# Kernel tuning notes

Hardware: AMD Instinct MI355X
Metric: run time of the kernel (lower is better)

## Reference

```python
import jax, jax.numpy as jnp
import numpy as np
from jax import lax

C = 512   # n_feat == Cn == Cdim (forced by DA_conv/CA_layer consistency)
H, W = 16, 32  # reshape_codebooks(512)
K = 3     # kernel_size
RED = 8   # reduction


def _lrelu(x):
    return jax.nn.leaky_relu(x, 0.1)


def _conv1x1(x, w, b=None):
    # x: (B,C,H,W), w: (O,C) -- torch Conv2d(.,.,1) weight squeezed
    y = jnp.einsum('oc,bchw->bohw', w, x)
    if b is not None:
        y = y + b[None, :, None, None]
    return y


def _conv3x3(x, w, b):
    # x: (B,C,H,W), w: (O,C,3,3) OIHW, padding=k//2 == SAME for odd k
    y = lax.conv_general_dilated(x, w, (1, 1), 'SAME',
                                 dimension_numbers=('NCHW', 'OIHW', 'NCHW'))
    return y + b[None, :, None, None]


def _da_conv(c, deg, kw1, kw2, pw, pb, caw1, caw2):
    # per-channel dynamic kernels from degradation vectors: (Cn, K*K)
    kern = (_lrelu(deg @ kw1.T) @ kw2.T).reshape(C, 1, K, K)
    # depthwise conv, groups = b1*c1 = C (b1 == 1)
    out = lax.conv_general_dilated(c, kern, (1, 1), 'SAME',
                                   feature_group_count=C,
                                   dimension_numbers=('NCHW', 'OIHW', 'NCHW'))
    out = _lrelu(out)
    out = _conv1x1(out, pw, pb)
    # CA_layer: deg reshaped to (1, Cn, 16, 32), channel attention, deg * att
    dr = deg.reshape(1, C, H, W)
    att = jax.nn.sigmoid(_conv1x1(_lrelu(_conv1x1(dr, caw1)), caw2))
    return out + dr * att


def setup_inputs() -> dict:
    key = jax.random.key(0)
    ks = jax.random.split(key, 16)
    n = lambda i, shape, s=0.05: jax.random.normal(ks[i], shape, dtype=jnp.float32) * s
    return dict(
        c=jax.random.normal(ks[0], (1, C, H, W), dtype=jnp.float32),
        deg=jax.random.normal(ks[1], (C, C), dtype=jnp.float32) * 0.1,
        k1_w1=n(2, (C, C)), k1_w2=n(3, (K * K, C)),
        p1_w=n(4, (C, C)), p1_b=jnp.zeros((C,), jnp.float32),
        ca1_w1=n(5, (C // RED, C)), ca1_w2=n(6, (C, C // RED)),
        conv1_w=n(7, (C, C, K, K)), conv1_b=jnp.zeros((C,), jnp.float32),
        k2_w1=n(8, (C, C)), k2_w2=n(9, (K * K, C)),
        p2_w=n(10, (C, C)), p2_b=jnp.zeros((C,), jnp.float32),
        ca2_w1=n(11, (C // RED, C)), ca2_w2=n(12, (C, C // RED)),
        conv2_w=n(13, (C, C, K, K)), conv2_b=jnp.zeros((C,), jnp.float32),
    )


def reference(c, deg, k1_w1, k1_w2, p1_w, p1_b, ca1_w1, ca1_w2,
              conv1_w, conv1_b, k2_w1, k2_w2, p2_w, p2_b,
              ca2_w1, ca2_w2, conv2_w, conv2_b):
    out = _lrelu(_da_conv(c, deg, k1_w1, k1_w2, p1_w, p1_b, ca1_w1, ca1_w2))
    out = _lrelu(_conv3x3(out, conv1_w, conv1_b))
    out = _lrelu(_da_conv(out, deg, k2_w1, k2_w2, p2_w, p2_b, ca2_w1, ca2_w2))
    return _conv3x3(out, conv2_w, conv2_b) + c
```

## Files before the change

kernel.cpp:

```cpp
#include <hip/hip_runtime.h>
#include <hip/hip_bf16.h>

typedef __attribute__((ext_vector_type(8))) unsigned short ushort8;
typedef __attribute__((ext_vector_type(8))) __bf16 bf16x8;
typedef __attribute__((ext_vector_type(4))) float f32x4;
typedef __attribute__((ext_vector_type(4))) unsigned short ushort4v;

__device__ __forceinline__ float lrelu_f(float v){ return v > 0.f ? v : 0.1f*v; }

__device__ __forceinline__ unsigned short f2bf(float v){
  unsigned u = __float_as_uint(v);
  unsigned r = (u + 0x7fffu + ((u>>16)&1u)) >> 16;
  return (unsigned short)r;
}
__device__ __forceinline__ float bf2f(unsigned short u){
  return __uint_as_float(((unsigned)u)<<16);
}

__device__ __forceinline__ void packq(const float* __restrict__ s,
                                      unsigned short* __restrict__ d, int i){
  const float4 v = ((const float4*)s)[i];
  ushort4v o; o.x=f2bf(v.x); o.y=f2bf(v.y); o.z=f2bf(v.z); o.w=f2bf(v.w);
  *(ushort4v*)(d + (size_t)i*4) = o;
}

__global__ __launch_bounds__(256) void k_pack_all(
  const float* __restrict__ k1_w1, const float* __restrict__ k2_w1,
  const float* __restrict__ p1_w,  const float* __restrict__ p2_w,
  const float* __restrict__ ca1_w1,const float* __restrict__ ca1_w2,
  const float* __restrict__ ca2_w1,const float* __restrict__ ca2_w2,
  const float* __restrict__ deg,   const float* __restrict__ conv1_w,
  const float* __restrict__ conv2_w,
  unsigned short* __restrict__ K1B, unsigned short* __restrict__ K2B,
  unsigned short* __restrict__ P1B, unsigned short* __restrict__ P2B,
  unsigned short* __restrict__ CA1A,unsigned short* __restrict__ CA1B,
  unsigned short* __restrict__ CA2A,unsigned short* __restrict__ CA2B,
  unsigned short* __restrict__ DEGB,unsigned short* __restrict__ DEGT,
  unsigned short* __restrict__ WB1, unsigned short* __restrict__ WB2){
  int i = blockIdx.x*256 + threadIdx.x;
  if (i < 65536){ packq(k1_w1, K1B, i); return; } i -= 65536;
  if (i < 65536){ packq(k2_w1, K2B, i); return; } i -= 65536;
  if (i < 65536){ packq(p1_w,  P1B, i); return; } i -= 65536;
  if (i < 65536){ packq(p2_w,  P2B, i); return; } i -= 65536;
  if (i < 8192){ packq(ca1_w1, CA1A, i); return; } i -= 8192;
  if (i < 8192){ packq(ca1_w2, CA1B, i); return; } i -= 8192;
  if (i < 8192){ packq(ca2_w1, CA2A, i); return; } i -= 8192;
  if (i < 8192){ packq(ca2_w2, CA2B, i); return; } i -= 8192;
  if (i < 65536){ packq(deg, DEGB, i); return; } i -= 65536;
  if (i < 65536){
    const int j = i*4; const int p = j>>9, c = j&511;
    ushort4v o;
    o.x = f2bf(deg[(size_t)(c+0)*512 + p]);
    o.y = f2bf(deg[(size_t)(c+1)*512 + p]);
    o.z = f2bf(deg[(size_t)(c+2)*512 + p]);
    o.w = f2bf(deg[(size_t)(c+3)*512 + p]);
    *(ushort4v*)(DEGT + (size_t)j) = o;
    return;
  } i -= 65536;
  if (i < 589824){
    const int o_ = i/1152; const int r4 = (i - o_*1152)*4;
    const int t = r4>>9; const int ci = r4&511;
    const float* s = conv1_w + (size_t)o_*4608;
    ushort4v o;
    o.x = f2bf(s[(ci+0)*9 + t]); o.y = f2bf(s[(ci+1)*9 + t]);
    o.z = f2bf(s[(ci+2)*9 + t]); o.w = f2bf(s[(ci+3)*9 + t]);
    *(ushort4v*)(WB1 + (size_t)o_*4608 + r4) = o;
    return;
  } i -= 589824;
  if (i < 589824){
    const int o_ = i/1152; const int r4 = (i - o_*1152)*4;
    const int t = r4>>9; const int ci = r4&511;
    const float* s = conv2_w + (size_t)o_*4608;
    ushort4v o;
    o.x = f2bf(s[(ci+0)*9 + t]); o.y = f2bf(s[(ci+1)*9 + t]);
    o.z = f2bf(s[(ci+2)*9 + t]); o.w = f2bf(s[(ci+3)*9 + t]);
    *(ushort4v*)(WB2 + (size_t)o_*4608 + r4) = o;
  }
}

__device__ __forceinline__ void gemm64(
    const unsigned short* __restrict__ A, const unsigned short* __restrict__ Bt,
    int m0, int n0, int K, int tid,
    unsigned short* lA, unsigned short* lB, f32x4 acc[2][2]){
  const int wid = tid>>6, lane = tid&63;
  const int srow = tid>>2, skb = tid&3;
  const unsigned short* gA = A  + (size_t)(m0+srow)*K + skb*8;
  const unsigned short* gB = Bt + (size_t)(n0+srow)*K + skb*8;
  const int soff = srow*32 + 8*(skb ^ (srow&3));
  const int wr = (wid>>1)*32, wc = (wid&1)*32;
  const int l15 = lane&15, lkb = lane>>4;
  int aoff[2], boff[2];
  #pragma unroll
  for (int s=0;s<2;s++){
    const int Ra = wr + s*16 + l15;
    aoff[s] = Ra*32 + 8*(lkb ^ (Ra&3));
    const int Rb = wc + s*16 + l15;
    boff[s] = Rb*32 + 8*(lkb ^ (Rb&3));
  }
  const int nst = K>>5;
  ushort8 ra = *(const ushort8*)gA;
  ushort8 rb = *(const ushort8*)gB;
  *(ushort8*)(lA + soff) = ra;
  *(ushort8*)(lB + soff) = rb;
  if (nst > 1){ ra = *(const ushort8*)(gA+32); rb = *(const ushort8*)(gB+32); }
  __syncthreads();
  for (int st=0; st<nst; ++st){
    const int cur = (st&1)*2048;
    bf16x8 af[2], bfr[2];
    #pragma unroll
    for (int s=0;s<2;s++){
      af[s]  = *(const bf16x8*)(lA + cur + aoff[s]);
      bfr[s] = *(const bf16x8*)(lB + cur + boff[s]);
    }
    if (st+1 < nst){
      const int nxt = ((st+1)&1)*2048;
      *(ushort8*)(lA + nxt + soff) = ra;
      *(ushort8*)(lB + nxt + soff) = rb;
      if (st+2 < nst){
        ra = *(const ushort8*)(gA + (size_t)(st+2)*32);
        rb = *(const ushort8*)(gB + (size_t)(st+2)*32);
      }
    }
    #pragma unroll
    for (int mi=0;mi<2;mi++)
      #pragma unroll
      for (int ni=0;ni<2;ni++)
        acc[mi][ni] = __builtin_amdgcn_mfma_f32_16x16x32_bf16(af[mi], bfr[ni], acc[mi][ni], 0,0,0);
    __syncthreads();
  }
}

__global__ __launch_bounds__(256) void k_mgemm_pre(
    const unsigned short* __restrict__ DEGB, const unsigned short* __restrict__ DEGT,
    const unsigned short* __restrict__ K1B,  const unsigned short* __restrict__ K2B,
    const unsigned short* __restrict__ CA1A, const unsigned short* __restrict__ CA2A,
    float* __restrict__ TMP1, float* __restrict__ TMP2,
    unsigned short* __restrict__ HID1, unsigned short* __restrict__ HID2){
  const int z = blockIdx.z;
  if (z >= 2 && blockIdx.y != 0) return;
  const unsigned short* A  = (z < 2) ? DEGB : DEGT;
  const unsigned short* Bt = (z==0) ? K1B : (z==1) ? K2B : (z==2) ? CA1A : CA2A;
  __shared__ unsigned short lA[4096], lB[4096];
  const int tid = threadIdx.x;
  const int m0 = blockIdx.x*64, n0 = blockIdx.y*64;
  f32x4 acc[2][2] = {};
  gemm64(A, Bt, m0, n0, 512, tid, lA, lB, acc);

  const int wid = tid>>6, lane = tid&63;
  const int wr = (wid>>1)*32, wc = (wid&1)*32;
  const int l15 = lane&15, lkb = lane>>4;
  #pragma unroll
  for (int mi=0;mi<2;mi++)
    #pragma unroll
    for (int ni=0;ni<2;ni++){
      const int row = m0 + wr + mi*16 + lkb*4;
      const int col = n0 + wc + ni*16 + l15;
      #pragma unroll
      for (int r=0;r<4;r++){
        const float v = lrelu_f(acc[mi][ni][r]);
        if (z==0)      TMP1[(size_t)(row+r)*512 + col] = v;
        else if (z==1) TMP2[(size_t)(row+r)*512 + col] = v;
        else if (z==2) HID1[(size_t)(row+r)*64 + col] = f2bf(v);
        else           HID2[(size_t)(row+r)*64 + col] = f2bf(v);
      }
    }
}

__global__ __launch_bounds__(256) void k_kern_att(
    const float* __restrict__ TMP1, const float* __restrict__ TMP2,
    const float* __restrict__ kw2a, const float* __restrict__ kw2b,
    const unsigned short* __restrict__ CA1B, const unsigned short* __restrict__ CA2B,
    const unsigned short* __restrict__ HID1, const unsigned short* __restrict__ HID2,
    float* __restrict__ kern0, float* __restrict__ kern1,
    float* __restrict__ ATT1, float* __restrict__ ATT2){
  const int z = blockIdx.z;
  const int tid = threadIdx.x;
  if (z < 2){
    const float* tmp  = z ? TMP2 : TMP1;
    const float* kw2  = z ? kw2b : kw2a;
    float* kern       = z ? kern1 : kern0;
    const int i = blockIdx.x*4 + (tid>>6);
    const int lane = tid&63;
    float acc[9];
    #pragma unroll
    for (int q=0;q<9;q++) acc[q]=0.f;
    for (int j=lane; j<512; j+=64){
      const float t = tmp[i*512 + j];
      #pragma unroll
      for (int q=0;q<9;q++) acc[q] += t*kw2[q*512 + j];
    }
    #pragma unroll
    for (int q=0;q<9;q++){
      float v = acc[q];
      #pragma unroll
      for (int off=32; off>0; off>>=1) v += __shfl_down(v, off);
      if (lane==0) kern[i*9+q] = v;
    }
  } else {
    if (blockIdx.x >= 64) return;
    const unsigned short* A  = (z==2) ? CA1B : CA2B;
    const unsigned short* Bt = (z==2) ? HID1 : HID2;
    float* ATT               = (z==2) ? ATT1 : ATT2;
    __shared__ unsigned short lA[4096], lB[4096];
    const int m0 = (blockIdx.x>>3)*64, n0 = (blockIdx.x&7)*64;
    f32x4 acc[2][2] = {};
    gemm64(A, Bt, m0, n0, 64, tid, lA, lB, acc);
    const int wid = tid>>6, lane = tid&63;
    const int wr = (wid>>1)*32, wc = (wid&1)*32;
    const int l15 = lane&15, lkb = lane>>4;
    #pragma unroll
    for (int mi=0;mi<2;mi++)
      #pragma unroll
      for (int ni=0;ni<2;ni++){
        const int row = m0 + wr + mi*16 + lkb*4;
        const int col = n0 + wc + ni*16 + l15;
        #pragma unroll
        for (int r=0;r<4;r++)
          ATT[(size_t)(row+r)*512 + col] = 1.f/(1.f + expf(-acc[mi][ni][r]));
      }
  }
}

__global__ __launch_bounds__(512) void k_dwconv(const float* __restrict__ x,
    const float* __restrict__ kern, unsigned short* __restrict__ yt){
  const int c = blockIdx.x;
  const int p = threadIdx.x;
  const int iy = p>>5, ix = p&31;
  __shared__ float plane[18*34];
  for (int i=p;i<18*34;i+=512) plane[i]=0.f;
  __syncthreads();
  plane[(iy+1)*34 + ix+1] = x[c*512 + p];
  __syncthreads();
  const float* kp = kern + c*9;
  float s = 0.f;
  #pragma unroll
  for (int dy=0;dy<3;dy++)
    #pragma unroll
    for (int dx=0;dx<3;dx++)
      s += plane[(iy+dy)*34 + ix+dx]*kp[dy*3+dx];
  yt[(size_t)p*512 + c] = f2bf(lrelu_f(s));
}

__global__ __launch_bounds__(512) void k_dwconv_red(const unsigned short* __restrict__ part,
    const float* __restrict__ bias, const float* __restrict__ kern,
    unsigned short* __restrict__ yt, int nchunks){
  const int c = blockIdx.x;
  const int p = threadIdx.x;
  const int iy = p>>5, ix = p&31;
  __shared__ float plane[18*34];
  for (int i=p;i<18*34;i+=512) plane[i]=0.f;
  __syncthreads();
  if (p < 128){
    const float b = bias[c];
    float4 a4 = {b,b,b,b};
    for (int s=0;s<nchunks;s++){
      const ushort4v v = ((const ushort4v*)(part + (size_t)s*262144 + c*512))[p];
      a4.x += bf2f(v.x); a4.y += bf2f(v.y); a4.z += bf2f(v.z); a4.w += bf2f(v.w);
    }
    a4.x = lrelu_f(a4.x); a4.y = lrelu_f(a4.y);
    a4.z = lrelu_f(a4.z); a4.w = lrelu_f(a4.w);
    const int px0 = p*4;
    float* dst = &plane[((px0>>5)+1)*34 + (px0&31)+1];
    dst[0]=a4.x; dst[1]=a4.y; dst[2]=a4.z; dst[3]=a4.w;
  }
  __syncthreads();
  const float* kp = kern + c*9;
  float s = 0.f;
  #pragma unroll
  for (int dy=0;dy<3;dy++)
    #pragma unroll
    for (int dx=0;dx<3;dx++)
      s += plane[(iy+dy)*34 + ix+dx]*kp[dy*3+dx];
  yt[(size_t)p*512 + c] = f2bf(lrelu_f(s));
}

__global__ __launch_bounds__(256) void k_pw(
    const unsigned short* __restrict__ A, const unsigned short* __restrict__ Bt,
    const float* __restrict__ bias,
    const float* __restrict__ E1, const float* __restrict__ E2,
    unsigned short* __restrict__ XT){
  __shared__ unsigned short lA[2][1024], lB[2][1024];
  __shared__ float tile[32][33];
  const int tid = threadIdx.x;
  const int wid = tid>>6, lane = tid&63;
  const int M0 = blockIdx.x*32, N0 = blockIdx.y*32;

  const int half = tid>>7;
  const int st_ = tid&127;
  const int srow = st_>>2, skb = st_&3;
  const unsigned short* gS = (half ? Bt + (size_t)(N0+srow)*512
                                   : A  + (size_t)(M0+srow)*512) + skb*8;
  unsigned short (*lS)[1024] = half ? lB : lA;
  const int soff = srow*32 + 8*(skb ^ (srow&3));

  const int wr = (wid>>1)*16, wc = (wid&1)*16;
  const int l15 = lane&15, lkb = lane>>4;
  const int Ra = wr + l15, Rb = wc + l15;
  const int aoff = Ra*32 + 8*(lkb ^ (Ra&3));
  const int boff = Rb*32 + 8*(lkb ^ (Rb&3));

  f32x4 acc = {};
  ushort8 r0 = *(const ushort8*)gS;
  *(ushort8*)(&lS[0][soff]) = r0;
  r0 = *(const ushort8*)(gS+32);
  __syncthreads();
  for (int st=0; st<16; ++st){
    const int cur = st&1;
    const bf16x8 af = *(const bf16x8*)(&lA[cur][aoff]);
    const bf16x8 bf = *(const bf16x8*)(&lB[cur][boff]);
    if (st+1 < 16){
      *(ushort8*)(&lS[cur^1][soff]) = r0;
      if (st+2 < 16) r0 = *(const ushort8*)(gS + (size_t)(st+2)*32);
    }
    acc = __builtin_amdgcn_mfma_f32_16x16x32_bf16(af, bf, acc, 0,0,0);
    __syncthreads();
  }

  #pragma unroll
  for (int r=0;r<4;r++){
    const int rl = wr + lkb*4 + r;
    const int cl = wc + l15;
    const int rr = M0 + rl, col = N0 + cl;
    float v = acc[r] + bias[rr] + E1[(size_t)rr*512+col]*E2[(size_t)rr*512+col];
    tile[rl][cl] = lrelu_f(v);
  }
  __syncthreads();
  const int pr = tid>>3, q = tid&7;
  ushort4v o;
  o.x = f2bf(tile[q*4+0][pr]); o.y = f2bf(tile[q*4+1][pr]);
  o.z = f2bf(tile[q*4+2][pr]); o.w = f2bf(tile[q*4+3][pr]);
  *(ushort4v*)(XT + (size_t)(N0+pr)*512 + M0 + q*4) = o;
}

template<int KCH>
__global__ __launch_bounds__(256) void k_mfma_conv(
    const unsigned short* __restrict__ WB,
    const unsigned short* __restrict__ XT,
    unsigned short* __restrict__ part){
  __shared__ unsigned short lA[2][4096];
  __shared__ unsigned short lB[2][8192];
  const int tid = threadIdx.x;
  const int wid = tid>>6, lane = tid&63;
  const int m0 = blockIdx.x*64, n0 = blockIdx.y*128;
  const int k0 = blockIdx.z*KCH;

  const int srow = tid>>2, skb = tid&3;
  const unsigned short* gA = WB + (size_t)(m0+srow)*4608 + k0 + skb*8;
  const int brow1 = srow + 64;
  const int p0 = n0 + srow, p1 = n0 + brow1;
  const int py0 = p0>>5, px0 = p0&31, py1 = p1>>5, px1 = p1&31;
  const int s7 = srow&7;
  const int soffA0 = srow*64 + 8*(skb ^ s7);
  const int soffA1 = srow*64 + 8*((skb+4) ^ s7);
  const int soffB00 = soffA0,            soffB01 = soffA1;
  const int soffB10 = brow1*64 + 8*(skb ^ s7);
  const int soffB11 = brow1*64 + 8*((skb+4) ^ s7);

  const int wr = (wid>>1)*32, wc = (wid&1)*64;
  const int l15 = lane&15, lkb = lane>>4;
  int aoff[2][2], boff[4][2];
  #pragma unroll
  for (int s=0;s<2;s++){
    const int Ra = wr + s*16 + l15;
    #pragma unroll
    for (int h=0;h<2;h++) aoff[s][h] = Ra*64 + 8*((lkb+4*h) ^ (Ra&7));
  }
  #pragma unroll
  for (int u=0;u<4;u++){
    const int Rb = wc + u*16 + l15;
    #pragma unroll
    for (int h=0;h<2;h++) boff[u][h] = Rb*64 + 8*((lkb+4*h) ^ (Rb&7));
  }

  auto ldB = [&](int st, int py, int px, ushort8& lo, ushort8& hi){
    const int k = k0 + st*64;
    const int t = k>>9;
    const int dy = t/3, dx = t - dy*3;
    const int yy = py + dy - 1, xx = px + dx - 1;
    lo = (ushort8){}; hi = (ushort8){};
    if ((unsigned)yy < 16u && (unsigned)xx < 32u){
      const unsigned short* b = XT + (size_t)(yy*32+xx)*512 + (k&511) + skb*8;
      lo = *(const ushort8*)b; hi = *(const ushort8*)(b+32);
    }
  };

  constexpr int NST = KCH/64;
  f32x4 acc[2][4] = {};
  ushort8 ra0 = *(const ushort8*)gA;
  ushort8 ra1 = *(const ushort8*)(gA+32);
  ushort8 b00,b01,b10,b11;
  ldB(0, py0, px0, b00, b01);
  ldB(0, py1, px1, b10, b11);
  *(ushort8*)(&lA[0][soffA0]) = ra0;  *(ushort8*)(&lA[0][soffA1]) = ra1;
  *(ushort8*)(&lB[0][soffB00]) = b00; *(ushort8*)(&lB[0][soffB01]) = b01;
  *(ushort8*)(&lB[0][soffB10]) = b10; *(ushort8*)(&lB[0][soffB11]) = b11;
  if (NST > 1){
    ra0 = *(const ushort8*)(gA+64); ra1 = *(const ushort8*)(gA+96);
    ldB(1, py0, px0, b00, b01);
    ldB(1, py1, px1, b10, b11);
  }
  __syncthreads();
  for (int st=0; st<NST; ++st){
    const int cur = st&1;
    bf16x8 af[2][2], bfr[4][2];
    #pragma unroll
    for (int s=0;s<2;s++)
      #pragma unroll
      for (int h=0;h<2;h++) af[s][h] = *(const bf16x8*)(&lA[cur][aoff[s][h]]);
    #pragma unroll
    for (int u=0;u<4;u++)
      #pragma unroll
      for (int h=0;h<2;h++) bfr[u][h] = *(const bf16x8*)(&lB[cur][boff[u][h]]);
    if (st+1 < NST){
      const int nxt = cur^1;
      *(ushort8*)(&lA[nxt][soffA0]) = ra0;  *(ushort8*)(&lA[nxt][soffA1]) = ra1;
      *(ushort8*)(&lB[nxt][soffB00]) = b00; *(ushort8*)(&lB[nxt][soffB01]) = b01;
      *(ushort8*)(&lB[nxt][soffB10]) = b10; *(ushort8*)(&lB[nxt][soffB11]) = b11;
      if (st+2 < NST){
        ra0 = *(const ushort8*)(gA + (size_t)(st+2)*64);
        ra1 = *(const ushort8*)(gA + (size_t)(st+2)*64 + 32);
        ldB(st+2, py0, px0, b00, b01);
        ldB(st+2, py1, px1, b10, b11);
      }
    }
    #pragma unroll
    for (int h=0;h<2;h++)
      #pragma unroll
      for (int s=0;s<2;s++)
        #pragma unroll
        for (int u=0;u<4;u++)
          acc[s][u] = __builtin_amdgcn_mfma_f32_16x16x32_bf16(af[s][h], bfr[u][h], acc[s][u], 0,0,0);
    __syncthreads();
  }

  unsigned short* pbase = part + (size_t)blockIdx.z*262144;
  #pragma unroll
  for (int s=0;s<2;s++)
    #pragma unroll
    for (int u=0;u<4;u++){
      const int row = m0 + wr + s*16 + lkb*4;
      const int col = n0 + wc + u*16 + l15;
      #pragma unroll
      for (int r=0;r<4;r++)
        pbase[(size_t)(row+r)*512 + col] = f2bf(acc[s][u][r]);
    }
}

__global__ __launch_bounds__(256) void k_reduce_final(const unsigned short* __restrict__ part,
    const float* __restrict__ bias, const float* __restrict__ res,
    float* __restrict__ y, int nchunks){
  const int i = blockIdx.x*256 + threadIdx.x;
  const int o = i>>7;
  const float b = bias[o];
  float4 a4 = {b,b,b,b};
  for (int s=0;s<nchunks;s++){
    const ushort4v v = ((const ushort4v*)part)[(size_t)s*65536 + i];
    a4.x += bf2f(v.x); a4.y += bf2f(v.y); a4.z += bf2f(v.z); a4.w += bf2f(v.w);
  }
  const float4 rv = ((const float4*)res)[i];
  a4.x += rv.x; a4.y += rv.y; a4.z += rv.z; a4.w += rv.w;
  ((float4*)y)[i] = a4;
}

extern "C" void kernel_launch(void* const* d_in, const int* in_sizes, int n_in,
                              void* d_out, int out_size, void* d_ws, size_t ws_size,
                              hipStream_t stream) {
  (void)in_sizes; (void)n_in; (void)out_size; (void)ws_size;
  const float* xin    = (const float*)d_in[0];
  const float* deg    = (const float*)d_in[1];
  const float* k1_w1  = (const float*)d_in[2];
  const float* k1_w2  = (const float*)d_in[3];
  const float* p1_w   = (const float*)d_in[4];
  const float* p1_b   = (const float*)d_in[5];
  const float* ca1_w1 = (const float*)d_in[6];
  const float* ca1_w2 = (const float*)d_in[7];
  const float* conv1_w= (const float*)d_in[8];
  const float* conv1_b= (const float*)d_in[9];
  const float* k2_w1  = (const float*)d_in[10];
  const float* k2_w2  = (const float*)d_in[11];
  const float* p2_w   = (const float*)d_in[12];
  const float* p2_b   = (const float*)d_in[13];
  const float* ca2_w1 = (const float*)d_in[14];
  const float* ca2_w2 = (const float*)d_in[15];
  const float* conv2_w= (const float*)d_in[16];
  const float* conv2_b= (const float*)d_in[17];
  float* out = (float*)d_out;

  const int NS = 18;

  float* ws = (float*)d_ws;
  unsigned short* PART = (unsigned short*)ws;
  ws += (size_t)NS*131072;
  float* TMP1 = (float*)PART;
  float* TMP2 = TMP1 + 262144;
  unsigned short* HID1 = (unsigned short*)(TMP2 + 262144);
  unsigned short* HID2 = HID1 + 32768;
  float* KERN1 = ws;  ws += 4608;
  float* KERN2 = ws;  ws += 4608;
  float* ATT1  = ws;  ws += 262144;
  float* ATT2  = ws;  ws += 262144;
  unsigned short* DEGB = (unsigned short*)ws; ws += 131072;
  unsigned short* DEGT = (unsigned short*)ws; ws += 131072;
  unsigned short* K1B  = (unsigned short*)ws; ws += 131072;
  unsigned short* K2B  = (unsigned short*)ws; ws += 131072;
  unsigned short* P1B  = (unsigned short*)ws; ws += 131072;
  unsigned short* P2B  = (unsigned short*)ws; ws += 131072;
  unsigned short* CA1A = (unsigned short*)ws; ws += 16384;
  unsigned short* CA1B = (unsigned short*)ws; ws += 16384;
  unsigned short* CA2A = (unsigned short*)ws; ws += 16384;
  unsigned short* CA2B = (unsigned short*)ws; ws += 16384;
  unsigned short* DWLT = (unsigned short*)ws; ws += 131072;
  unsigned short* XT   = (unsigned short*)ws; ws += 131072;
  unsigned short* WB1  = (unsigned short*)ws; ws += 1179648;
  unsigned short* WB2  = (unsigned short*)ws; ws += 1179648;

  k_pack_all<<<6272,256,0,stream>>>(k1_w1,k2_w1,p1_w,p2_w,
      ca1_w1,ca1_w2,ca2_w1,ca2_w2, deg, conv1_w, conv2_w,
      K1B,K2B,P1B,P2B, CA1A,CA1B,CA2A,CA2B, DEGB,DEGT, WB1,WB2);

  k_mgemm_pre<<<dim3(8,8,4),256,0,stream>>>(DEGB,DEGT, K1B,K2B, CA1A,CA2A,
      TMP1,TMP2, HID1,HID2);
  k_kern_att<<<dim3(128,1,4),256,0,stream>>>(TMP1,TMP2, k1_w2,k2_w2,
      CA1B,CA2B, HID1,HID2, KERN1,KERN2, ATT1,ATT2);

  k_dwconv<<<512,512,0,stream>>>(xin, KERN1, DWLT);
  k_pw<<<dim3(16,16),256,0,stream>>>(P1B, DWLT, p1_b, deg, ATT1, XT);
  k_mfma_conv<256><<<dim3(8,4,18),256,0,stream>>>(WB1, XT, PART);
  k_dwconv_red<<<512,512,0,stream>>>(PART, conv1_b, KERN2, DWLT, NS);
  k_pw<<<dim3(16,16),256,0,stream>>>(P2B, DWLT, p2_b, deg, ATT2, XT);
  k_mfma_conv<256><<<dim3(8,4,18),256,0,stream>>>(WB2, XT, PART);
  k_reduce_final<<<256,256,0,stream>>>(PART, conv2_b, xin, out, NS);
}
```

Baseline: 85.13 us.

## Fuse degradation-kernel and channel-attention prep GEMMs into one kernel

Merges the two precompute kernels into a single launch. The dynamic-kernel branch reduces each 64-column GEMM tile against kw2 in the epilogue and writes per-column-chunk partials, which the depthwise conv kernels then sum. The channel-attention branch keeps the hidden layer in swizzled shared memory and runs the second GEMM plus sigmoid in the same block. This removes one launch and the fp32 TMP/HID round trips through global memory. In exchange the grid shrinks to 144 blocks, and the attention blocks serially loop over all 512 output rows.

```diff
diff --git a/kernel.cpp b/kernel.cpp
--- a/kernel.cpp
+++ b/kernel.cpp
@@ -130,125 +130,181 @@
   }
 }
 
-__global__ __launch_bounds__(256) void k_mgemm_pre(
+__global__ __launch_bounds__(256) void k_prep(
     const unsigned short* __restrict__ DEGB, const unsigned short* __restrict__ DEGT,
     const unsigned short* __restrict__ K1B,  const unsigned short* __restrict__ K2B,
     const unsigned short* __restrict__ CA1A, const unsigned short* __restrict__ CA2A,
-    float* __restrict__ TMP1, float* __restrict__ TMP2,
-    unsigned short* __restrict__ HID1, unsigned short* __restrict__ HID2){
-  const int z = blockIdx.z;
-  if (z >= 2 && blockIdx.y != 0) return;
-  const unsigned short* A  = (z < 2) ? DEGB : DEGT;
-  const unsigned short* Bt = (z==0) ? K1B : (z==1) ? K2B : (z==2) ? CA1A : CA2A;
+    const unsigned short* __restrict__ CA1B, const unsigned short* __restrict__ CA2B,
+    const float* __restrict__ kw2a, const float* __restrict__ kw2b,
+    float* __restrict__ KP1, float* __restrict__ KP2,
+    float* __restrict__ ATT1, float* __restrict__ ATT2){
   __shared__ unsigned short lA[4096], lB[4096];
+  __shared__ float kp[2][64][9];
+  __shared__ unsigned short hid[4096];
+  int bid = blockIdx.x;
   const int tid = threadIdx.x;
-  const int m0 = blockIdx.x*64, n0 = blockIdx.y*64;
-  f32x4 acc[2][2] = {};
-  gemm64(A, Bt, m0, n0, 512, tid, lA, lB, acc);
-
   const int wid = tid>>6, lane = tid&63;
-  const int wr = (wid>>1)*32, wc = (wid&1)*32;
   const int l15 = lane&15, lkb = lane>>4;
-  #pragma unroll
-  for (int mi=0;mi<2;mi++)
+
+  if (bid < 128){
+    const int b  = bid>>6;
+    const int r6 = bid&63;
+    const int it = r6>>3, jc = r6&7;
+    const unsigned short* Bt = b ? K2B : K1B;
+    const float* kw2 = b ? kw2b : kw2a;
+    float* KP = b ? KP2 : KP1;
+    f32x4 acc[2][2] = {};
+    gemm64(DEGB, Bt, it*64, jc*64, 512, tid, lA, lB, acc);
+
+    const int wr = (wid>>1)*32, wcl = wid&1;
+    const int col0 = wcl*32 + l15, col1 = col0 + 16;
+    float w0[9], w1[9];
+    #pragma unroll
+    for (int t=0;t<9;t++){
+      w0[t] = kw2[t*512 + jc*64 + col0];
+      w1[t] = kw2[t*512 + jc*64 + col1];
+    }
+    #pragma unroll
+    for (int mi=0;mi<2;mi++)
+      #pragma unroll
+      for (int r=0;r<4;r++){
+        const float v0 = lrelu_f(acc[mi][0][r]);
+        const float v1 = lrelu_f(acc[mi][1][r]);
+        const int row = wr + mi*16 + lkb*4 + r;
+        #pragma unroll
+        for (int t=0;t<9;t++){
+          float p = v0*w0[t] + v1*w1[t];
+          p += __shfl_xor(p,1); p += __shfl_xor(p,2);
+          p += __shfl_xor(p,4); p += __shfl_xor(p,8);
+          if (l15==0) kp[wcl][row][t] = p;
+        }
+      }
+    __syncthreads();
+    for (int i = tid; i < 576; i += 256){
+      const int row = i/9, t = i - row*9;
+      KP[((size_t)jc*512 + it*64 + row)*9 + t] = kp[0][row][t] + kp[1][row][t];
+    }
+  } else {
+    bid -= 128;
+    const int b  = bid>>3;
+    const int pt = bid&7;
+    const unsigned short* CAa = b ? CA2A : CA1A;
+    const unsigned short* CAb = b ? CA2B : CA1B;
+    float* ATT = b ? ATT2 : ATT1;
+    f32x4 acc[2][2] = {};
+    gemm64(DEGT, CAa, pt*64, 0, 512, tid, lA, lB, acc);
+
+    {
+      const int wr = (wid>>1)*32, wc = (wid&1)*32;
+      #pragma unroll
+      for (int mi=0;mi<2;mi++)
+        #pragma unroll
+        for (int ni=0;ni<2;ni++)
+          #pragma unroll
+          for (int r=0;r<4;r++){
+            const int row = wr + mi*16 + lkb*4 + r;
+            const int col = wc + ni*16 + l15;
+            hid[row*64 + 8*((col>>3) ^ (row&7)) + (col&7)] = f2bf(lrelu_f(acc[mi][ni][r]));
+          }
+    }
+    __syncthreads();
+
+    const int wr = (wid>>1)*32, wc = (wid&1)*32;
+    int boff2[2][2], aoff2[2][2];
     #pragma unroll
     for (int ni=0;ni<2;ni++){
-      const int row = m0 + wr + mi*16 + lkb*4;
-      const int col = n0 + wc + ni*16 + l15;
-      #pragma unroll
-      for (int r=0;r<4;r++){
-        const float v = lrelu_f(acc[mi][ni][r]);
-        if (z==0)      TMP1[(size_t)(row+r)*512 + col] = v;
-        else if (z==1) TMP2[(size_t)(row+r)*512 + col] = v;
-        else if (z==2) HID1[(size_t)(row+r)*64 + col] = f2bf(v);
-        else           HID2[(size_t)(row+r)*64 + col] = f2bf(v);
+      const int Rb = wc + ni*16 + l15;
+      #pragma unroll
+      for (int h=0;h<2;h++) boff2[ni][h] = Rb*64 + 8*((h*4 + lkb) ^ (Rb&7));
+    }
+    #pragma unroll
+    for (int mi=0;mi<2;mi++){
+      const int Ra = wr + mi*16 + l15;
+      #pragma unroll
+      for (int h=0;h<2;h++) aoff2[mi][h] = Ra*64 + 8*((h*4 + lkb) ^ (Ra&7));
+    }
+    bf16x8 bf2[2][2];
+    #pragma unroll
+    for (int ni=0;ni<2;ni++)
+      #pragma unroll
+      for (int h=0;h<2;h++) bf2[ni][h] = *(const bf16x8*)(hid + boff2[ni][h]);
+
+    const int arow = tid>>2, akb0 = (tid&3)*2;
+    for (int m0=0; m0<512; m0+=64){
+      __syncthreads();
+      #pragma unroll
+      for (int kk=0;kk<2;kk++){
+        const int kb = akb0+kk;
+        *(ushort8*)(lA + arow*64 + 8*(kb ^ (arow&7))) =
+          *(const ushort8*)(CAb + (size_t)(m0+arow)*64 + kb*8);
       }
-    }
-}
-
-__global__ __launch_bounds__(256) void k_kern_att(
-    const float* __restrict__ TMP1, const float* __restrict__ TMP2,
-    const float* __restrict__ kw2a, const float* __restrict__ kw2b,
-    const unsigned short* __restrict__ CA1B, const unsigned short* __restrict__ CA2B,
-    const unsigned short* __restrict__ HID1, const unsigned short* __restrict__ HID2,
-    float* __restrict__ kern0, float* __restrict__ kern1,
-    float* __restrict__ ATT1, float* __restrict__ ATT2){
-  const int z = blockIdx.z;
-  const int tid = threadIdx.x;
-  if (z < 2){
-    const float* tmp  = z ? TMP2 : TMP1;
-    const float* kw2  = z ? kw2b : kw2a;
-    float* kern       = z ? kern1 : kern0;
-    const int i = blockIdx.x*4 + (tid>>6);
-    const int lane = tid&63;
-    float acc[9];
-    #pragma unroll
-    for (int q=0;q<9;q++) acc[q]=0.f;
-    for (int j=lane; j<512; j+=64){
-      const float t = tmp[i*512 + j];
-      #pragma unroll
-      for (int q=0;q<9;q++) acc[q] += t*kw2[q*512 + j];
-    }
-    #pragma unroll
-    for (int q=0;q<9;q++){
-      float v = acc[q];
-      #pragma unroll
-      for (int off=32; off>0; off>>=1) v += __shfl_down(v, off);
-      if (lane==0) kern[i*9+q] = v;
-    }
-  } else {
-    if (blockIdx.x >= 64) return;
-    const unsigned short* A  = (z==2) ? CA1B : CA2B;
-    const unsigned short* Bt = (z==2) ? HID1 : HID2;
-    float* ATT               = (z==2) ? ATT1 : ATT2;
-    __shared__ unsigned short lA[4096], lB[4096];
-    const int m0 = (blockIdx.x>>3)*64, n0 = (blockIdx.x&7)*64;
-    f32x4 acc[2][2] = {};
-    gemm64(A, Bt, m0, n0, 64, tid, lA, lB, acc);
-    const int wid = tid>>6, lane = tid&63;
-    const int wr = (wid>>1)*32, wc = (wid&1)*32;
-    const int l15 = lane&15, lkb = lane>>4;
-    #pragma unroll
-    for (int mi=0;mi<2;mi++)
-      #pragma unroll
-      for (int ni=0;ni<2;ni++){
-        const int row = m0 + wr + mi*16 + lkb*4;
-        const int col = n0 + wc + ni*16 + l15;
+      __syncthreads();
+      f32x4 a2[2][2] = {};
+      #pragma unroll
+      for (int h=0;h<2;h++)
         #pragma unroll
-        for (int r=0;r<4;r++)
-          ATT[(size_t)(row+r)*512 + col] = 1.f/(1.f + expf(-acc[mi][ni][r]));
-      }
+        for (int mi=0;mi<2;mi++){
+          const bf16x8 af2 = *(const bf16x8*)(lA + aoff2[mi][h]);
+          #pragma unroll
+          for (int ni=0;ni<2;ni++)
+            a2[mi][ni] = __builtin_amdgcn_mfma_f32_16x16x32_bf16(af2, bf2[ni][h], a2[mi][ni], 0,0,0);
+        }
+      #pragma unroll
+      for (int mi=0;mi<2;mi++)
+        #pragma unroll
+        for (int ni=0;ni<2;ni++){
+          #pragma unroll
+          for (int r=0;r<4;r++){
+            const int row = m0 + wr + mi*16 + lkb*4 + r;
+            const int col = pt*64 + wc + ni*16 + l15;
+            ATT[(size_t)row*512 + col] = 1.f/(1.f + expf(-a2[mi][ni][r]));
+          }
+        }
+    }
   }
 }
 
 __global__ __launch_bounds__(512) void k_dwconv(const float* __restrict__ x,
-    const float* __restrict__ kern, unsigned short* __restrict__ yt){
+    const float* __restrict__ KP, unsigned short* __restrict__ yt){
   const int c = blockIdx.x;
   const int p = threadIdx.x;
   const int iy = p>>5, ix = p&31;
   __shared__ float plane[18*34];
+  __shared__ float ks[9];
   for (int i=p;i<18*34;i+=512) plane[i]=0.f;
+  if (p < 9){
+    float s = 0.f;
+    #pragma unroll
+    for (int jc=0;jc<8;jc++) s += KP[((size_t)jc*512 + c)*9 + p];
+    ks[p] = s;
+  }
   __syncthreads();
   plane[(iy+1)*34 + ix+1] = x[c*512 + p];
   __syncthreads();
-  const float* kp = kern + c*9;
   float s = 0.f;
   #pragma unroll
   for (int dy=0;dy<3;dy++)
     #pragma unroll
     for (int dx=0;dx<3;dx++)
-      s += plane[(iy+dy)*34 + ix+dx]*kp[dy*3+dx];
+      s += plane[(iy+dy)*34 + ix+dx]*ks[dy*3+dx];
   yt[(size_t)p*512 + c] = f2bf(lrelu_f(s));
 }
 
 __global__ __launch_bounds__(512) void k_dwconv_red(const unsigned short* __restrict__ part,
-    const float* __restrict__ bias, const float* __restrict__ kern,
+    const float* __restrict__ bias, const float* __restrict__ KP,
     unsigned short* __restrict__ yt, int nchunks){
   const int c = blockIdx.x;
   const int p = threadIdx.x;
   const int iy = p>>5, ix = p&31;
   __shared__ float plane[18*34];
+  __shared__ float ks[9];
   for (int i=p;i<18*34;i+=512) plane[i]=0.f;
+  if (p < 9){
+    float s = 0.f;
+    #pragma unroll
+    for (int jc=0;jc<8;jc++) s += KP[((size_t)jc*512 + c)*9 + p];
+    ks[p] = s;
+  }
   __syncthreads();
   if (p < 128){
     const float b = bias[c];
@@ -264,13 +320,12 @@
     dst[0]=a4.x; dst[1]=a4.y; dst[2]=a4.z; dst[3]=a4.w;
   }
   __syncthreads();
-  const float* kp = kern + c*9;
   float s = 0.f;
   #pragma unroll
   for (int dy=0;dy<3;dy++)
     #pragma unroll
     for (int dx=0;dx<3;dx++)
-      s += plane[(iy+dy)*34 + ix+dx]*kp[dy*3+dx];
+      s += plane[(iy+dy)*34 + ix+dx]*ks[dy*3+dx];
   yt[(size_t)p*512 + c] = f2bf(lrelu_f(s));
 }
 
@@ -491,14 +546,10 @@
   float* ws = (float*)d_ws;
   unsigned short* PART = (unsigned short*)ws;
   ws += (size_t)NS*131072;
-  float* TMP1 = (float*)PART;
-  float* TMP2 = TMP1 + 262144;
-  unsigned short* HID1 = (unsigned short*)(TMP2 + 262144);
-  unsigned short* HID2 = HID1 + 32768;
-  float* KERN1 = ws;  ws += 4608;
-  float* KERN2 = ws;  ws += 4608;
-  float* ATT1  = ws;  ws += 262144;
-  float* ATT2  = ws;  ws += 262144;
+  float* KP1  = ws;  ws += 36864;
+  float* KP2  = ws;  ws += 36864;
+  float* ATT1 = ws;  ws += 262144;
+  float* ATT2 = ws;  ws += 262144;
   unsigned short* DEGB = (unsigned short*)ws; ws += 131072;
   unsigned short* DEGT = (unsigned short*)ws; ws += 131072;
   unsigned short* K1B  = (unsigned short*)ws; ws += 131072;
@@ -518,15 +569,13 @@
       ca1_w1,ca1_w2,ca2_w1,ca2_w2, deg, conv1_w, conv2_w,
       K1B,K2B,P1B,P2B, CA1A,CA1B,CA2A,CA2B, DEGB,DEGT, WB1,WB2);
 
-  k_mgemm_pre<<<dim3(8,8,4),256,0,stream>>>(DEGB,DEGT, K1B,K2B, CA1A,CA2A,
-      TMP1,TMP2, HID1,HID2);
-  k_kern_att<<<dim3(128,1,4),256,0,stream>>>(TMP1,TMP2, k1_w2,k2_w2,
-      CA1B,CA2B, HID1,HID2, KERN1,KERN2, ATT1,ATT2);
-
-  k_dwconv<<<512,512,0,stream>>>(xin, KERN1, DWLT);
+  k_prep<<<144,256,0,stream>>>(DEGB,DEGT, K1B,K2B, CA1A,CA2A, CA1B,CA2B,
+      k1_w2,k2_w2, KP1,KP2, ATT1,ATT2);
+
+  k_dwconv<<<512,512,0,stream>>>(xin, KP1, DWLT);
   k_pw<<<dim3(16,16),256,0,stream>>>(P1B, DWLT, p1_b, deg, ATT1, XT);
   k_mfma_conv<256><<<dim3(8,4,18),256,0,stream>>>(WB1, XT, PART);
-  k_dwconv_red<<<512,512,0,stream>>>(PART, conv1_b, KERN2, DWLT, NS);
+  k_dwconv_red<<<512,512,0,stream>>>(PART, conv1_b, KP2, DWLT, NS);
   k_pw<<<dim3(16,16),256,0,stream>>>(P2B, DWLT, p2_b, deg, ATT2, XT);
   k_mfma_conv<256><<<dim3(8,4,18),256,0,stream>>>(WB2, XT, PART);
   k_reduce_final<<<256,256,0,stream>>>(PART, conv2_b, xin, out, NS);
```

Measured after the change: 88.55 us. +4.0%, slower.

## Use padded activation layout and direct global-to-LDS loads in 3x3 conv GEMM

Applied to the files above, without the earlier changes.

The transposed activation buffer becomes zero-padded (18x34 slots), so the 3x3 implicit-GEMM conv needs no boundary checks. The border slots are zeroed by the first dwconv kernel, and the buffer reuses the K1B workspace. The conv kernel now stages A and B tiles with global_load_lds (async copy straight to LDS, XOR swizzle applied on the source address) instead of register-staged loads. This removes register pressure and explicit LDS stores. The trade-off is a changed prefetch depth (one stage ahead) and reliance on K1B not being needed after the pre-GEMM.

```diff
diff --git a/kernel.cpp b/kernel.cpp
--- a/kernel.cpp
+++ b/kernel.cpp
@@ -15,6 +15,12 @@
 }
 __device__ __forceinline__ float bf2f(unsigned short u){
   return __uint_as_float(((unsigned)u)<<16);
+}
+
+__device__ __forceinline__ void gload16(const void* g, void* l){
+  __builtin_amdgcn_global_load_lds(
+    (const __attribute__((address_space(1))) unsigned int*)g,
+    (__attribute__((address_space(3))) unsigned int*)l, 16, 0, 0);
 }
 
 __device__ __forceinline__ void packq(const float* __restrict__ s,
@@ -222,10 +228,24 @@
 }
 
 __global__ __launch_bounds__(512) void k_dwconv(const float* __restrict__ x,
-    const float* __restrict__ kern, unsigned short* __restrict__ yt){
+    const float* __restrict__ kern, unsigned short* __restrict__ yt,
+    unsigned short* __restrict__ XTP){
   const int c = blockIdx.x;
   const int p = threadIdx.x;
   const int iy = p>>5, ix = p&31;
+  {
+    const int idx = blockIdx.x*512 + p;
+    if (idx < 12800){
+      const int si = idx>>7, wi = idx&127;
+      int slot;
+      if (si < 34) slot = si;
+      else if (si < 68) slot = 578 + (si-34);
+      else if (si < 84) slot = (si-67)*34;
+      else slot = (si-83)*34 + 33;
+      ushort4v z = {};
+      *(ushort4v*)(XTP + (size_t)slot*512 + wi*4) = z;
+    }
+  }
   __shared__ float plane[18*34];
   for (int i=p;i<18*34;i+=512) plane[i]=0.f;
   __syncthreads();
@@ -278,7 +298,7 @@
     const unsigned short* __restrict__ A, const unsigned short* __restrict__ Bt,
     const float* __restrict__ bias,
     const float* __restrict__ E1, const float* __restrict__ E2,
-    unsigned short* __restrict__ XT){
+    unsigned short* __restrict__ XTP){
   __shared__ unsigned short lA[2][1024], lB[2][1024];
   __shared__ float tile[32][33];
   const int tid = threadIdx.x;
@@ -326,35 +346,42 @@
   }
   __syncthreads();
   const int pr = tid>>3, q = tid&7;
+  const int p = N0 + pr;
+  const int slot = ((p>>5)+1)*34 + (p&31) + 1;
   ushort4v o;
   o.x = f2bf(tile[q*4+0][pr]); o.y = f2bf(tile[q*4+1][pr]);
   o.z = f2bf(tile[q*4+2][pr]); o.w = f2bf(tile[q*4+3][pr]);
-  *(ushort4v*)(XT + (size_t)(N0+pr)*512 + M0 + q*4) = o;
+  *(ushort4v*)(XTP + (size_t)slot*512 + M0 + q*4) = o;
 }
 
 template<int KCH>
 __global__ __launch_bounds__(256) void k_mfma_conv(
     const unsigned short* __restrict__ WB,
-    const unsigned short* __restrict__ XT,
+    const unsigned short* __restrict__ XTP,
     unsigned short* __restrict__ part){
-  __shared__ unsigned short lA[2][4096];
-  __shared__ unsigned short lB[2][8192];
+  __shared__ __attribute__((aligned(16))) unsigned short lA[2][4096];
+  __shared__ __attribute__((aligned(16))) unsigned short lB[2][8192];
   const int tid = threadIdx.x;
   const int wid = tid>>6, lane = tid&63;
   const int m0 = blockIdx.x*64, n0 = blockIdx.y*128;
   const int k0 = blockIdx.z*KCH;
 
-  const int srow = tid>>2, skb = tid&3;
-  const unsigned short* gA = WB + (size_t)(m0+srow)*4608 + k0 + skb*8;
-  const int brow1 = srow + 64;
-  const int p0 = n0 + srow, p1 = n0 + brow1;
-  const int py0 = p0>>5, px0 = p0&31, py1 = p1>>5, px1 = p1&31;
-  const int s7 = srow&7;
-  const int soffA0 = srow*64 + 8*(skb ^ s7);
-  const int soffA1 = srow*64 + 8*((skb+4) ^ s7);
-  const int soffB00 = soffA0,            soffB01 = soffA1;
-  const int soffB10 = brow1*64 + 8*(skb ^ s7);
-  const int soffB11 = brow1*64 + 8*((skb+4) ^ s7);
+  const int wrow = wid*8 + (lane>>3);
+  const int clin = lane&7;
+  const unsigned short* asrc[2];
+  #pragma unroll
+  for (int j=0;j<2;j++){
+    const int r = j*32 + wrow;
+    asrc[j] = WB + (size_t)(m0+r)*4608 + k0 + (clin ^ (r&7))*8;
+  }
+  int bpy[4], bpx[4], bchk[4];
+  #pragma unroll
+  for (int j=0;j<4;j++){
+    const int r = j*32 + wrow;
+    const int pp = n0 + r;
+    bpy[j] = pp>>5; bpx[j] = pp&31;
+    bchk[j] = (clin ^ (r&7))*8;
+  }
 
   const int wr = (wid>>1)*32, wc = (wid&1)*64;
   const int l15 = lane&15, lkb = lane>>4;
@@ -372,36 +399,30 @@
     for (int h=0;h<2;h++) boff[u][h] = Rb*64 + 8*((lkb+4*h) ^ (Rb&7));
   }
 
-  auto ldB = [&](int st, int py, int px, ushort8& lo, ushort8& hi){
+  auto stage = [&](int buf, int st){
+    #pragma unroll
+    for (int j=0;j<2;j++)
+      gload16(asrc[j] + st*64, &lA[buf][j*2048 + wid*512]);
     const int k = k0 + st*64;
     const int t = k>>9;
     const int dy = t/3, dx = t - dy*3;
-    const int yy = py + dy - 1, xx = px + dx - 1;
-    lo = (ushort8){}; hi = (ushort8){};
-    if ((unsigned)yy < 16u && (unsigned)xx < 32u){
-      const unsigned short* b = XT + (size_t)(yy*32+xx)*512 + (k&511) + skb*8;
-      lo = *(const ushort8*)b; hi = *(const ushort8*)(b+32);
+    const int kc = k & 511;
+    #pragma unroll
+    for (int j=0;j<4;j++){
+      const int slot = (bpy[j]+dy)*34 + bpx[j]+dx;
+      gload16(XTP + (size_t)slot*512 + kc + bchk[j],
+              &lB[buf][j*2048 + wid*512]);
     }
   };
 
   constexpr int NST = KCH/64;
   f32x4 acc[2][4] = {};
-  ushort8 ra0 = *(const ushort8*)gA;
-  ushort8 ra1 = *(const ushort8*)(gA+32);
-  ushort8 b00,b01,b10,b11;
-  ldB(0, py0, px0, b00, b01);
-  ldB(0, py1, px1, b10, b11);
-  *(ushort8*)(&lA[0][soffA0]) = ra0;  *(ushort8*)(&lA[0][soffA1]) = ra1;
-  *(ushort8*)(&lB[0][soffB00]) = b00; *(ushort8*)(&lB[0][soffB01]) = b01;
-  *(ushort8*)(&lB[0][soffB10]) = b10; *(ushort8*)(&lB[0][soffB11]) = b11;
-  if (NST > 1){
-    ra0 = *(const ushort8*)(gA+64); ra1 = *(const ushort8*)(gA+96);
-    ldB(1, py0, px0, b00, b01);
-    ldB(1, py1, px1, b10, b11);
-  }
-  __syncthreads();
+  stage(0, 0);
+  __syncthreads();
+  #pragma unroll
   for (int st=0; st<NST; ++st){
     const int cur = st&1;
+    if (st+1 < NST) stage(cur^1, st+1);
     bf16x8 af[2][2], bfr[4][2];
     #pragma unroll
     for (int s=0;s<2;s++)
@@ -411,18 +432,6 @@
     for (int u=0;u<4;u++)
       #pragma unroll
       for (int h=0;h<2;h++) bfr[u][h] = *(const bf16x8*)(&lB[cur][boff[u][h]]);
-    if (st+1 < NST){
-      const int nxt = cur^1;
-      *(ushort8*)(&lA[nxt][soffA0]) = ra0;  *(ushort8*)(&lA[nxt][soffA1]) = ra1;
-      *(ushort8*)(&lB[nxt][soffB00]) = b00; *(ushort8*)(&lB[nxt][soffB01]) = b01;
-      *(ushort8*)(&lB[nxt][soffB10]) = b10; *(ushort8*)(&lB[nxt][soffB11]) = b11;
-      if (st+2 < NST){
-        ra0 = *(const ushort8*)(gA + (size_t)(st+2)*64);
-        ra1 = *(const ushort8*)(gA + (size_t)(st+2)*64 + 32);
-        ldB(st+2, py0, px0, b00, b01);
-        ldB(st+2, py1, px1, b10, b11);
-      }
-    }
     #pragma unroll
     for (int h=0;h<2;h++)
       #pragma unroll
@@ -503,6 +512,7 @@
   unsigned short* DEGT = (unsigned short*)ws; ws += 131072;
   unsigned short* K1B  = (unsigned short*)ws; ws += 131072;
   unsigned short* K2B  = (unsigned short*)ws; ws += 131072;
+  unsigned short* XTP  = K1B;
   unsigned short* P1B  = (unsigned short*)ws; ws += 131072;
   unsigned short* P2B  = (unsigned short*)ws; ws += 131072;
   unsigned short* CA1A = (unsigned short*)ws; ws += 16384;
@@ -510,7 +520,6 @@
   unsigned short* CA2A = (unsigned short*)ws; ws += 16384;
   unsigned short* CA2B = (unsigned short*)ws; ws += 16384;
   unsigned short* DWLT = (unsigned short*)ws; ws += 131072;
-  unsigned short* XT   = (unsigned short*)ws; ws += 131072;
   unsigned short* WB1  = (unsigned short*)ws; ws += 1179648;
   unsigned short* WB2  = (unsigned short*)ws; ws += 1179648;
 
@@ -523,11 +532,11 @@
   k_kern_att<<<dim3(128,1,4),256,0,stream>>>(TMP1,TMP2, k1_w2,k2_w2,
       CA1B,CA2B, HID1,HID2, KERN1,KERN2, ATT1,ATT2);
 
-  k_dwconv<<<512,512,0,stream>>>(xin, KERN1, DWLT);
-  k_pw<<<dim3(16,16),256,0,stream>>>(P1B, DWLT, p1_b, deg, ATT1, XT);
-  k_mfma_conv<256><<<dim3(8,4,18),256,0,stream>>>(WB1, XT, PART);
+  k_dwconv<<<512,512,0,stream>>>(xin, KERN1, DWLT, XTP);
+  k_pw<<<dim3(16,16),256,0,stream>>>(P1B, DWLT, p1_b, deg, ATT1, XTP);
+  k_mfma_conv<256><<<dim3(8,4,18),256,0,stream>>>(WB1, XTP, PART);
   k_dwconv_red<<<512,512,0,stream>>>(PART, conv1_b, KERN2, DWLT, NS);
-  k_pw<<<dim3(16,16),256,0,stream>>>(P2B, DWLT, p2_b, deg, ATT2, XT);
-  k_mfma_conv<256><<<dim3(8,4,18),256,0,stream>>>(WB2, XT, PART);
+  k_pw<<<dim3(16,16),256,0,stream>>>(P2B, DWLT, p2_b, deg, ATT2, XTP);
+  k_mfma_conv<256><<<dim3(8,4,18),256,0,stream>>>(WB2, XTP, PART);
   k_reduce_final<<<256,256,0,stream>>>(PART, conv2_b, xin, out, NS);
 }
```

Measured after the change: 86.21 us. About the same (+1.3%).
